# Optimization experiments

Hardware: AMD Instinct MI355X
Metric: run time of the kernel (lower is better)

The kernel has to match this reference:

```python
import jax, jax.numpy as jnp
import numpy as np

IN_F, HID, OUT = 128, 128, 32
N_NODES, N_EDGES, N_GRAPHS = 100000, 1600000, 64


def gcn_conv(x, W, b, src, dst, n):
    """PyG-style GCNConv: add self-loops, symmetric deg^-1/2 norm, linear, scatter-add."""
    h = x @ W  # [N, F_out]
    loop = jnp.arange(n)
    src_f = jnp.concatenate([src, loop])
    dst_f = jnp.concatenate([dst, loop])
    deg = jax.ops.segment_sum(jnp.ones_like(dst_f, dtype=x.dtype), dst_f, num_segments=n)
    dinv = jax.lax.rsqrt(jnp.maximum(deg, 1.0))  # deg >= 1 because of self-loops
    norm = dinv[src_f] * dinv[dst_f]             # [E+N]
    msg = h[src_f] * norm[:, None]               # gather + scale, [E+N, F_out]
    out = jax.ops.segment_sum(msg, dst_f, num_segments=n)  # scatter-add
    return out + b


def setup_inputs() -> dict:
    key = jax.random.key(0)
    ks = jax.random.split(key, 10)
    x = jax.random.normal(ks[0], (N_NODES, IN_F), dtype=jnp.float32)
    edge_index = jax.random.randint(ks[1], (2, N_EDGES), 0, N_NODES, dtype=jnp.int64)
    batch = jnp.sort(jax.random.randint(ks[2], (N_NODES,), 0, N_GRAPHS, dtype=jnp.int64))

    def glorot(k, fi, fo):
        s = np.sqrt(6.0 / (fi + fo)).astype(np.float32)
        return jax.random.uniform(k, (fi, fo), dtype=jnp.float32, minval=-s, maxval=s)

    return {
        "x": x,
        "edge_index": edge_index,
        "batch": batch,
        "num_graphs": N_GRAPHS,
        "W1": glorot(ks[3], IN_F, HID), "b1": jnp.zeros((HID,), jnp.float32),
        "W2": glorot(ks[4], HID, HID), "b2": jnp.zeros((HID,), jnp.float32),
        "W3": glorot(ks[5], HID, OUT), "b3": jnp.zeros((OUT,), jnp.float32),
    }


def reference(x, edge_index, batch, num_graphs, W1, b1, W2, b2, W3, b3):
    n = x.shape[0]
    src, dst = edge_index[0], edge_index[1]
    # Dropout is identity in eval mode.
    h = jax.nn.relu(gcn_conv(x, W1, b1, src, dst, n))
    h = jax.nn.relu(gcn_conv(h, W2, b2, src, dst, n))
    h = gcn_conv(h, W3, b3, src, dst, n)  # [N, OUT]
    # global_mean_pool over batch ids
    sums = jax.ops.segment_sum(h, batch, num_segments=num_graphs)
    cnts = jax.ops.segment_sum(jnp.ones((n,), h.dtype), batch, num_segments=num_graphs)
    x_global = sums / jnp.maximum(cnts, 1.0)[:, None]
    return h, x_global
```

## Files before the change

### kernel.cpp

```cpp
#include <hip/hip_runtime.h>
#include <hip/hip_bf16.h>


typedef unsigned int uint32;
typedef short short8 __attribute__((ext_vector_type(8)));
typedef float f32x4 __attribute__((ext_vector_type(4)));

static __device__ __forceinline__ unsigned short f2bf(float f) {
    uint32 u = __float_as_uint(f);
    return (unsigned short)((u + 0x7fffu + ((u >> 16) & 1u)) >> 16);
}
static __device__ __forceinline__ float bf2f_lo(uint32 u) {
    return __uint_as_float(u << 16);
}
static __device__ __forceinline__ float bf2f_hi(uint32 u) {
    return __uint_as_float(u & 0xffff0000u);
}

__global__ __launch_bounds__(256) void initdeg_k(int* deg, int M) {
    int i = blockIdx.x * 256 + threadIdx.x;
    if (i < M) deg[i] = 1;
}

__global__ __launch_bounds__(256) void count_k(const int* __restrict__ dst, int E,
                                               int* __restrict__ deg) {
    int e = blockIdx.x * 256 + threadIdx.x;
    if (e < E) atomicAdd(&deg[__builtin_nontemporal_load(&dst[e])], 1);
}

__global__ __launch_bounds__(256) void mkdinv_k(const int* __restrict__ deg,
                                                float* __restrict__ dinv, int M) {
    int i = blockIdx.x * 256 + threadIdx.x;
    if (i < M) dinv[i] = rsqrtf((float)deg[i]);
}

__global__ __launch_bounds__(256) void scan1_k(const int* __restrict__ deg, int M,
                                               int* __restrict__ blksum) {
    __shared__ int sh[256];
    int i = blockIdx.x * 256 + threadIdx.x;
    int v = (i < M) ? deg[i] - 1 : 0;
    sh[threadIdx.x] = v;
    __syncthreads();
    for (int o = 128; o > 0; o >>= 1) {
        if (threadIdx.x < o) sh[threadIdx.x] += sh[threadIdx.x + o];
        __syncthreads();
    }
    if (threadIdx.x == 0) blksum[blockIdx.x] = sh[0];
}

__global__ __launch_bounds__(512) void scan2_k(int* __restrict__ blksum, int nb) {
    __shared__ int sh[512];
    int tid = threadIdx.x;
    int v = (tid < nb) ? blksum[tid] : 0;
    sh[tid] = v;
    __syncthreads();
    for (int o = 1; o < 512; o <<= 1) {
        int t = (tid >= o) ? sh[tid - o] : 0;
        __syncthreads();
        sh[tid] += t;
        __syncthreads();
    }
    if (tid < nb) blksum[tid] = sh[tid] - v;
}

__global__ __launch_bounds__(256) void scan3_k(const int* __restrict__ deg, int M,
                                               const int* __restrict__ blksum,
                                               int* __restrict__ rowptr,
                                               int* __restrict__ cursor) {
    __shared__ int sh[256];
    int tid = threadIdx.x;
    int i = blockIdx.x * 256 + tid;
    int v = (i < M) ? deg[i] - 1 : 0;
    sh[tid] = v;
    __syncthreads();
    for (int o = 1; o < 256; o <<= 1) {
        int t = (tid >= o) ? sh[tid - o] : 0;
        __syncthreads();
        sh[tid] += t;
        __syncthreads();
    }
    int excl = sh[tid] - v + blksum[blockIdx.x];
    if (i < M) {
        rowptr[i] = excl;
        cursor[i] = excl;
    }
    if (i == M - 1) rowptr[M] = excl + v;
}

#define FILL_CHUNK 4096
__global__ __launch_bounds__(256) void fill_rp_k(const int* __restrict__ src,
                                                 const int* __restrict__ dst,
                                                 int E, int M,
                                                 int* __restrict__ cursor,
                                                 int* __restrict__ col) {
    const int r = blockIdx.x & 7;
    const int chunk = blockIdx.x >> 3;
    const int lo = (int)(((long long)r * M) >> 3);
    const int hi = (int)(((long long)(r + 1) * M) >> 3);
    const int base = chunk * FILL_CHUNK;
    const int end = min(E, base + FILL_CHUNK);
    for (int e = base + (int)threadIdx.x; e < end; e += 256) {
        int d = __builtin_nontemporal_load(&dst[e]);
        int s = __builtin_nontemporal_load(&src[e]);
        if (d >= lo && d < hi) {
            int slot = atomicAdd(&cursor[d], 1);
            col[slot] = s;
        }
    }
}

__global__ __launch_bounds__(256) void cvt_k(const float* __restrict__ x,
                                             unsigned short* __restrict__ o,
                                             int n8) {
    int i = blockIdx.x * 256 + threadIdx.x;
    if (i >= n8) return;
    const float4* xp = (const float4*)x + (size_t)i * 2;
    float4 a = xp[0], b = xp[1];
    union { unsigned short us[8]; uint4 v; } u;
    u.us[0] = f2bf(a.x); u.us[1] = f2bf(a.y); u.us[2] = f2bf(a.z); u.us[3] = f2bf(a.w);
    u.us[4] = f2bf(b.x); u.us[5] = f2bf(b.y); u.us[6] = f2bf(b.z); u.us[7] = f2bf(b.w);
    *((uint4*)o + i) = u.v;
}

__global__ __launch_bounds__(256) void wt_k(const float* __restrict__ W,
                                            unsigned short* __restrict__ Wt,
                                            int N) {
    int idx = blockIdx.x * 256 + threadIdx.x;
    if (idx >= N * 128) return;
    int n = idx >> 7, k = idx & 127;
    Wt[idx] = f2bf(W[k * N + n]);
}

template <int NT>
__global__ __launch_bounds__(256) void mgemm_k(const unsigned short* __restrict__ A,
                                               const unsigned short* __restrict__ Wt,
                                               const float* __restrict__ dinv,
                                               unsigned short* __restrict__ C,
                                               int M, int nstrips) {
    constexpr int N = NT * 16;
    const int lane = threadIdx.x & 63;
    const int wid = threadIdx.x >> 6;
    const int r = lane & 15;
    const int g = lane >> 4;

    short8 wf[NT][4];
#pragma unroll
    for (int t = 0; t < NT; t++)
#pragma unroll
        for (int s = 0; s < 4; s++)
            wf[t][s] = *(const short8*)&Wt[(size_t)(t * 16 + r) * 128 + s * 32 + g * 8];

    const int stride = gridDim.x * 4;
    for (int strip = blockIdx.x * 4 + wid; strip < nstrips; strip += stride) {
        const int R = strip * 16;
        const int ar = min(R + r, M - 1);
        short8 af[4];
#pragma unroll
        for (int s = 0; s < 4; s++)
            af[s] = *(const short8*)&A[(size_t)ar * 128 + s * 32 + g * 8];
        f32x4 acc[NT];
#pragma unroll
        for (int t = 0; t < NT; t++) acc[t] = (f32x4){0.f, 0.f, 0.f, 0.f};
#pragma unroll
        for (int s = 0; s < 4; s++)
#pragma unroll
            for (int t = 0; t < NT; t++)
                acc[t] = __builtin_amdgcn_mfma_f32_16x16x32_bf16(
                    af[s], wf[t][s], acc[t], 0, 0, 0);
#pragma unroll
        for (int j = 0; j < 4; j++) {
            int row = R + 4 * g + j;
            if (row < M) {
                float dv = dinv[row];
#pragma unroll
                for (int t = 0; t < NT; t++)
                    C[(size_t)row * N + t * 16 + r] = f2bf(dv * acc[t][j]);
            }
        }
    }
}

__global__ __launch_bounds__(256) void agg128_k(const unsigned short* __restrict__ Hb,
                                                const int* __restrict__ rowptr,
                                                const int* __restrict__ col,
                                                const float* __restrict__ dinv,
                                                const float* __restrict__ bias,
                                                unsigned short* __restrict__ outb,
                                                int M, int relu) {
    int node = blockIdx.x * 4 + (threadIdx.x >> 6);
    if (node >= M) return;
    int lane = threadIdx.x & 63;
    const uint32* Hu = (const uint32*)Hb;
    uint32 su = Hu[(size_t)node * 64 + lane];
    float ax = bf2f_lo(su);
    float ay = bf2f_hi(su);
    const int s = rowptr[node], e = rowptr[node + 1];

    for (int base = s; base < e; base += 64) {
        int n = e - base;
        if (n > 64) n = 64;
        int cid = __builtin_nontemporal_load(&col[base + (lane < n ? lane : 0)]);
        int j = 0;
        for (; j + 8 <= n; j += 8) {
            int sj[8]; uint32 u[8];
#pragma unroll
            for (int k = 0; k < 8; k++) sj[k] = __shfl(cid, j + k);
#pragma unroll
            for (int k = 0; k < 8; k++) u[k] = Hu[(size_t)sj[k] * 64 + lane];
#pragma unroll
            for (int k = 0; k < 8; k++) {
                ax += bf2f_lo(u[k]);
                ay += bf2f_hi(u[k]);
            }
        }
        for (; j < n; j++) {
            int s0 = __shfl(cid, j);
            uint32 u0 = Hu[(size_t)s0 * 64 + lane];
            ax += bf2f_lo(u0);
            ay += bf2f_hi(u0);
        }
    }
    float dv = dinv[node];
    float2 bv = *(const float2*)&bias[lane * 2];
    float ox = fmaf(dv, ax, bv.x), oy = fmaf(dv, ay, bv.y);
    if (relu) { ox = fmaxf(ox, 0.f); oy = fmaxf(oy, 0.f); }
    uint32 pk = (uint32)f2bf(ox) | ((uint32)f2bf(oy) << 16);
    *(uint32*)&outb[(size_t)node * 128 + lane * 2] = pk;
}

__global__ __launch_bounds__(256) void agg32_k(const unsigned short* __restrict__ Hb,
                                               const int* __restrict__ rowptr,
                                               const int* __restrict__ col,
                                               const float* __restrict__ dinv,
                                               const float* __restrict__ bias,
                                               float* __restrict__ out, int M) {
    int node = blockIdx.x * 4 + (threadIdx.x >> 6);
    if (node >= M) return;
    int lane = threadIdx.x & 63;
    int f = lane & 31;
    int half = lane >> 5;
    float acc = 0.f;
    if (!half)
        acc = __uint_as_float(((uint32)Hb[(size_t)node * 32 + f]) << 16);
    const int s = rowptr[node], e = rowptr[node + 1];
    int i = s + half;
    for (; i + 6 < e; i += 8) {
        int s0 = __builtin_nontemporal_load(&col[i]);
        int s1 = __builtin_nontemporal_load(&col[i + 2]);
        int s2 = __builtin_nontemporal_load(&col[i + 4]);
        int s3 = __builtin_nontemporal_load(&col[i + 6]);
        float h0 = __uint_as_float(((uint32)Hb[(size_t)s0 * 32 + f]) << 16);
        float h1 = __uint_as_float(((uint32)Hb[(size_t)s1 * 32 + f]) << 16);
        float h2 = __uint_as_float(((uint32)Hb[(size_t)s2 * 32 + f]) << 16);
        float h3 = __uint_as_float(((uint32)Hb[(size_t)s3 * 32 + f]) << 16);
        acc += h0 + h1 + h2 + h3;
    }
    for (; i < e; i += 2) {
        int s0 = __builtin_nontemporal_load(&col[i]);
        acc += __uint_as_float(((uint32)Hb[(size_t)s0 * 32 + f]) << 16);
    }
    acc += __shfl_xor(acc, 32);
    if (!half) out[(size_t)node * 32 + f] = fmaf(dinv[node], acc, bias[f]);
}

__global__ __launch_bounds__(256) void pool_k(const float* __restrict__ h,
                                              const int* __restrict__ batch, int M,
                                              float* __restrict__ out) {
    int g = blockIdx.x;
    int lo, hi;
    {
        int l = 0, r = M;
        while (l < r) { int m = (l + r) >> 1; if (batch[m] < g) l = m + 1; else r = m; }
        lo = l;
    }
    {
        int l = lo, r = M;
        while (l < r) { int m = (l + r) >> 1; if (batch[m] < g + 1) l = m + 1; else r = m; }
        hi = l;
    }
    int f = threadIdx.x & 31;
    int chunk = threadIdx.x >> 5;
    float acc = 0.f;
    for (int i = lo + chunk; i < hi; i += 8) acc += h[(size_t)i * 32 + f];
    __shared__ float red[8][32];
    red[chunk][f] = acc;
    __syncthreads();
    if (threadIdx.x < 32) {
        float s = 0.f;
#pragma unroll
        for (int c = 0; c < 8; c++) s += red[c][f];
        out[g * 32 + f] = s / fmaxf((float)(hi - lo), 1.f);
    }
}

extern "C" void kernel_launch(void* const* d_in, const int* in_sizes, int n_in,
                              void* d_out, int out_size, void* d_ws, size_t ws_size,
                              hipStream_t stream) {
    const float* x   = (const float*)d_in[0];
    const int* ei    = (const int*)d_in[1];
    const int* batch = (const int*)d_in[2];
    const float* W1  = (const float*)d_in[4];
    const float* b1  = (const float*)d_in[5];
    const float* W2  = (const float*)d_in[6];
    const float* b2  = (const float*)d_in[7];
    const float* W3  = (const float*)d_in[8];
    const float* b3  = (const float*)d_in[9];

    const int M = in_sizes[0] / 128;
    const int E = in_sizes[1] / 2;
    const int G = 64;
    const int* srcp = ei;
    const int* dstp = ei + E;

    char* p = (char*)d_ws;
    auto carve = [&](size_t bytes) {
        void* r = (void*)p;
        p += (bytes + 255) & ~(size_t)255;
        return r;
    };
    int*   deg    = (int*)carve((size_t)M * 4);
    float* dinv   = (float*)carve((size_t)M * 4);
    int*   rowptr = (int*)carve((size_t)(M + 1) * 4);
    int*   cursor = (int*)carve((size_t)M * 4);
    int*   blksum = (int*)carve(512 * 4);
    int*   col    = (int*)carve((size_t)E * 4);
    unsigned short* Xb  = (unsigned short*)carve((size_t)M * 128 * 2);
    unsigned short* Hb  = (unsigned short*)carve((size_t)M * 128 * 2);
    unsigned short* Ob  = (unsigned short*)carve((size_t)M * 128 * 2);
    unsigned short* H3  = (unsigned short*)carve((size_t)M * 32 * 2);
    unsigned short* Wt1 = (unsigned short*)carve(128 * 128 * 2);
    unsigned short* Wt2 = (unsigned short*)carve(128 * 128 * 2);
    unsigned short* Wt3 = (unsigned short*)carve(32 * 128 * 2);

    float* outh = (float*)d_out;
    float* outg = outh + (size_t)M * 32;

    const int nbM = (M + 255) / 256;
    const int nbE = (E + 255) / 256;
    const int nstrips = (M + 15) / 16;
    const int gblk = (nstrips + 7) / 8;

    cvt_k<<<(M * 128 / 8 + 255) / 256, 256, 0, stream>>>(x, Xb, M * 128 / 8);
    initdeg_k<<<nbM, 256, 0, stream>>>(deg, M);
    count_k<<<nbE, 256, 0, stream>>>(dstp, E, deg);
    mkdinv_k<<<nbM, 256, 0, stream>>>(deg, dinv, M);
    scan1_k<<<nbM, 256, 0, stream>>>(deg, M, blksum);
    scan2_k<<<1, 512, 0, stream>>>(blksum, nbM);
    scan3_k<<<nbM, 256, 0, stream>>>(deg, M, blksum, rowptr, cursor);
    {
        const int nchunk = (E + FILL_CHUNK - 1) / FILL_CHUNK;
        fill_rp_k<<<nchunk * 8, 256, 0, stream>>>(srcp, dstp, E, M, cursor, col);
    }
    wt_k<<<(128 * 128 + 255) / 256, 256, 0, stream>>>(W1, Wt1, 128);
    wt_k<<<(128 * 128 + 255) / 256, 256, 0, stream>>>(W2, Wt2, 128);
    wt_k<<<(32 * 128 + 255) / 256, 256, 0, stream>>>(W3, Wt3, 32);

    mgemm_k<8><<<gblk, 256, 0, stream>>>(Xb, Wt1, dinv, Hb, M, nstrips);
    agg128_k<<<(M + 3) / 4, 256, 0, stream>>>(Hb, rowptr, col, dinv, b1, Ob, M, 1);
    mgemm_k<8><<<gblk, 256, 0, stream>>>(Ob, Wt2, dinv, Hb, M, nstrips);
    agg128_k<<<(M + 3) / 4, 256, 0, stream>>>(Hb, rowptr, col, dinv, b2, Ob, M, 1);
    mgemm_k<2><<<gblk, 256, 0, stream>>>(Ob, Wt3, dinv, H3, M, nstrips);
    agg32_k<<<(M + 3) / 4, 256, 0, stream>>>(H3, rowptr, col, dinv, b3, outh, M);
    pool_k<<<G, 256, 0, stream>>>(outh, batch, M, outg);
}
```

Baseline: 582.3 us.

## Build CSR via two-level bucketed counting sort instead of global atomics

Replaces the global-atomic degree count and the 8-pass range-filtered CSR fill with a bucketed radix approach. Edges are first histogrammed into buckets of 128 destination nodes using shared-memory atomics, then scattered into a packed bucket-ordered array (src | local dst << 20). Per-bucket kernels then compute degrees and fill the column array with localized atomics. This aims to cut random global atomic traffic and the repeated edge-list scans, at the cost of an extra E-sized buffer, more launches, and a packing scheme that limits src to 20 bits and M to 1024*128 nodes.

Measured after the change: 536.4 us. 1.09x faster.

```diff
diff --git a/kernel.cpp b/kernel.cpp
--- a/kernel.cpp
+++ b/kernel.cpp
@@ -6,6 +6,10 @@
 typedef short short8 __attribute__((ext_vector_type(8)));
 typedef float f32x4 __attribute__((ext_vector_type(4)));
 
+#define BSH 7
+#define MAXB 1024
+#define BCH 8192
+
 static __device__ __forceinline__ unsigned short f2bf(float f) {
     uint32 u = __float_as_uint(f);
     return (unsigned short)((u + 0x7fffu + ((u >> 16) & 1u)) >> 16);
@@ -17,15 +21,99 @@
     return __uint_as_float(u & 0xffff0000u);
 }
 
-__global__ __launch_bounds__(256) void initdeg_k(int* deg, int M) {
-    int i = blockIdx.x * 256 + threadIdx.x;
-    if (i < M) deg[i] = 1;
-}
-
-__global__ __launch_bounds__(256) void count_k(const int* __restrict__ dst, int E,
-                                               int* __restrict__ deg) {
-    int e = blockIdx.x * 256 + threadIdx.x;
-    if (e < E) atomicAdd(&deg[__builtin_nontemporal_load(&dst[e])], 1);
+__global__ __launch_bounds__(256) void zcnt_k(int* bcnt) {
+    bcnt[blockIdx.x * 256 + threadIdx.x] = 0;
+}
+
+__global__ __launch_bounds__(256) void bhist_k(const int* __restrict__ dst, int E,
+                                               int* __restrict__ bcnt) {
+    __shared__ int h[MAXB];
+    for (int i = threadIdx.x; i < MAXB; i += 256) h[i] = 0;
+    __syncthreads();
+    const int base = blockIdx.x * BCH;
+    const int end = min(E, base + BCH);
+    for (int e = base + (int)threadIdx.x; e < end; e += 256)
+        atomicAdd(&h[__builtin_nontemporal_load(&dst[e]) >> BSH], 1);
+    __syncthreads();
+    for (int i = threadIdx.x; i < MAXB; i += 256)
+        if (h[i]) atomicAdd(&bcnt[i], h[i]);
+}
+
+__global__ __launch_bounds__(256) void bscan_k(const int* __restrict__ bcnt,
+                                               int* __restrict__ bstart,
+                                               int* __restrict__ bcur, int B) {
+    __shared__ int tot[256];
+    const int tid = threadIdx.x;
+    int v[4];
+    int s = 0;
+#pragma unroll
+    for (int j = 0; j < 4; j++) {
+        int idx = tid * 4 + j;
+        v[j] = (idx < B) ? bcnt[idx] : 0;
+        s += v[j];
+    }
+    tot[tid] = s;
+    __syncthreads();
+    for (int o = 1; o < 256; o <<= 1) {
+        int t = (tid >= o) ? tot[tid - o] : 0;
+        __syncthreads();
+        tot[tid] += t;
+        __syncthreads();
+    }
+    int run = tot[tid] - s;
+#pragma unroll
+    for (int j = 0; j < 4; j++) {
+        int idx = tid * 4 + j;
+        if (idx < B) {
+            bstart[idx] = run;
+            bcur[idx] = run;
+            run += v[j];
+        }
+    }
+    if (tid == 255) bstart[B] = run;
+}
+
+__global__ __launch_bounds__(256) void bfill_k(const int* __restrict__ src,
+                                               const int* __restrict__ dst, int E,
+                                               int* __restrict__ bcur,
+                                               int* __restrict__ fifo) {
+    __shared__ int h[MAXB];
+    __shared__ int base[MAXB];
+    for (int i = threadIdx.x; i < MAXB; i += 256) h[i] = 0;
+    __syncthreads();
+    const int b0 = blockIdx.x * BCH;
+    const int end = min(E, b0 + BCH);
+    for (int e = b0 + (int)threadIdx.x; e < end; e += 256)
+        atomicAdd(&h[__builtin_nontemporal_load(&dst[e]) >> BSH], 1);
+    __syncthreads();
+    for (int i = threadIdx.x; i < MAXB; i += 256) {
+        int c = h[i];
+        base[i] = c ? atomicAdd(&bcur[i], c) : 0;
+        h[i] = 0;
+    }
+    __syncthreads();
+    for (int e = b0 + (int)threadIdx.x; e < end; e += 256) {
+        int d = __builtin_nontemporal_load(&dst[e]);
+        int s = __builtin_nontemporal_load(&src[e]);
+        int b = d >> BSH;
+        int off = base[b] + atomicAdd(&h[b], 1);
+        fifo[off] = s | ((d & 127) << 20);
+    }
+}
+
+__global__ __launch_bounds__(256) void bdeg_k(const int* __restrict__ fifo,
+                                              const int* __restrict__ bstart,
+                                              int* __restrict__ deg, int M) {
+    __shared__ int h[128];
+    const int t = threadIdx.x;
+    if (t < 128) h[t] = 0;
+    __syncthreads();
+    const int lo = bstart[blockIdx.x], hi = bstart[blockIdx.x + 1];
+    for (int i = lo + t; i < hi; i += 256)
+        atomicAdd(&h[fifo[i] >> 20], 1);
+    __syncthreads();
+    int node = (blockIdx.x << BSH) + t;
+    if (t < 128 && node < M) deg[node] = 1 + h[t];
 }
 
 __global__ __launch_bounds__(256) void mkdinv_k(const int* __restrict__ deg,
@@ -87,25 +175,17 @@
     if (i == M - 1) rowptr[M] = excl + v;
 }
 
-#define FILL_CHUNK 4096
-__global__ __launch_bounds__(256) void fill_rp_k(const int* __restrict__ src,
-                                                 const int* __restrict__ dst,
-                                                 int E, int M,
-                                                 int* __restrict__ cursor,
-                                                 int* __restrict__ col) {
-    const int r = blockIdx.x & 7;
-    const int chunk = blockIdx.x >> 3;
-    const int lo = (int)(((long long)r * M) >> 3);
-    const int hi = (int)(((long long)(r + 1) * M) >> 3);
-    const int base = chunk * FILL_CHUNK;
-    const int end = min(E, base + FILL_CHUNK);
-    for (int e = base + (int)threadIdx.x; e < end; e += 256) {
-        int d = __builtin_nontemporal_load(&dst[e]);
-        int s = __builtin_nontemporal_load(&src[e]);
-        if (d >= lo && d < hi) {
-            int slot = atomicAdd(&cursor[d], 1);
-            col[slot] = s;
-        }
+__global__ __launch_bounds__(256) void bcol_k(const int* __restrict__ fifo,
+                                              const int* __restrict__ bstart,
+                                              int* __restrict__ cursor,
+                                              int* __restrict__ col) {
+    const int lo = bstart[blockIdx.x], hi = bstart[blockIdx.x + 1];
+    const int nbase = blockIdx.x << BSH;
+    for (int i = lo + (int)threadIdx.x; i < hi; i += 256) {
+        int ev = fifo[i];
+        int node = nbase + (ev >> 20);
+        int slot = atomicAdd(&cursor[node], 1);
+        col[slot] = ev & 0xFFFFF;
     }
 }
 
@@ -311,6 +391,7 @@
     const int G = 64;
     const int* srcp = ei;
     const int* dstp = ei + E;
+    const int B = (M + 127) >> BSH;
 
     char* p = (char*)d_ws;
     auto carve = [&](size_t bytes) {
@@ -323,6 +404,10 @@
     int*   rowptr = (int*)carve((size_t)(M + 1) * 4);
     int*   cursor = (int*)carve((size_t)M * 4);
     int*   blksum = (int*)carve(512 * 4);
+    int*   bcnt   = (int*)carve(MAXB * 4);
+    int*   bstart = (int*)carve((MAXB + 1) * 4);
+    int*   bcur   = (int*)carve(MAXB * 4);
+    int*   fifo   = (int*)carve((size_t)E * 4);
     int*   col    = (int*)carve((size_t)E * 4);
     unsigned short* Xb  = (unsigned short*)carve((size_t)M * 128 * 2);
     unsigned short* Hb  = (unsigned short*)carve((size_t)M * 128 * 2);
@@ -336,21 +421,21 @@
     float* outg = outh + (size_t)M * 32;
 
     const int nbM = (M + 255) / 256;
-    const int nbE = (E + 255) / 256;
+    const int nbE = (E + BCH - 1) / BCH;
     const int nstrips = (M + 15) / 16;
     const int gblk = (nstrips + 7) / 8;
 
     cvt_k<<<(M * 128 / 8 + 255) / 256, 256, 0, stream>>>(x, Xb, M * 128 / 8);
-    initdeg_k<<<nbM, 256, 0, stream>>>(deg, M);
-    count_k<<<nbE, 256, 0, stream>>>(dstp, E, deg);
+    zcnt_k<<<MAXB / 256, 256, 0, stream>>>(bcnt);
+    bhist_k<<<nbE, 256, 0, stream>>>(dstp, E, bcnt);
+    bscan_k<<<1, 256, 0, stream>>>(bcnt, bstart, bcur, B);
+    bfill_k<<<nbE, 256, 0, stream>>>(srcp, dstp, E, bcur, fifo);
+    bdeg_k<<<B, 256, 0, stream>>>(fifo, bstart, deg, M);
     mkdinv_k<<<nbM, 256, 0, stream>>>(deg, dinv, M);
     scan1_k<<<nbM, 256, 0, stream>>>(deg, M, blksum);
     scan2_k<<<1, 512, 0, stream>>>(blksum, nbM);
     scan3_k<<<nbM, 256, 0, stream>>>(deg, M, blksum, rowptr, cursor);
-    {
-        const int nchunk = (E + FILL_CHUNK - 1) / FILL_CHUNK;
-        fill_rp_k<<<nchunk * 8, 256, 0, stream>>>(srcp, dstp, E, M, cursor, col);
-    }
+    bcol_k<<<B, 256, 0, stream>>>(fifo, bstart, cursor, col);
     wt_k<<<(128 * 128 + 255) / 256, 256, 0, stream>>>(W1, Wt1, 128);
     wt_k<<<(128 * 128 + 255) / 256, 256, 0, stream>>>(W2, Wt2, 128);
     wt_k<<<(32 * 128 + 255) / 256, 256, 0, stream>>>(W3, Wt3, 32);
```
